# Performance work log

Hardware: AMD Instinct MI355X
Metric: run time of the kernel (lower is better)

## Reference

```python
import jax, jax.numpy as jnp
import numpy as np

D = 256; NH = 8; NL = 4; NP = 4; HD = D // NH
SHAPES = np.array([[64, 64], [32, 32], [16, 16], [8, 8]], dtype=np.int32)  # (H, W) per level
LSI = np.array([0, 4096, 5120, 5376], dtype=np.int32)
B = 4; LQ = int(SHAPES.prod(axis=1).sum())  # 5440


def setup_inputs() -> dict:
    key = jax.random.key(0)
    ks = jax.random.split(key, 16)
    p = lambda i, shape, s=0.02: jax.random.normal(ks[i], shape, dtype=jnp.float32) * s
    return dict(
        src=jax.random.normal(ks[0], (B, LQ, D), dtype=jnp.float32),
        pos=jax.random.normal(ks[1], (B, LQ, D), dtype=jnp.float32),
        reference_points=jax.random.uniform(ks[2], (B, LQ, NL, 2), dtype=jnp.float32),
        spatial_shapes=jnp.asarray(SHAPES),
        level_start_index=jnp.asarray(LSI),
        Wv=p(3, (D, D)), bv=jnp.zeros((D,), jnp.float32),
        Woff=p(4, (D, NH * NL * NP * 2)), boff=p(5, (NH * NL * NP * 2,)),
        Wattn=p(6, (D, NH * NL * NP)), battn=p(7, (NH * NL * NP,)),
        Wout=p(8, (D, D)), bout=jnp.zeros((D,), jnp.float32),
        g1=jnp.ones((D,), jnp.float32), b1=jnp.zeros((D,), jnp.float32),
        W1=p(9, (D, D)), bb1=jnp.zeros((D,), jnp.float32),
        W2=p(10, (D, D)), bb2=jnp.zeros((D,), jnp.float32),
        g3=jnp.ones((D,), jnp.float32), b3=jnp.zeros((D,), jnp.float32),
    )


def _ln(x, g, b, eps=1e-5):
    m = jnp.mean(x, -1, keepdims=True)
    v = jnp.mean(jnp.square(x - m), -1, keepdims=True)
    return (x - m) * jax.lax.rsqrt(v + eps) * g + b


def _bilinear(vflat, Hl, Wl, loc):
    # vflat: [B, Hl*Wl, nh, hd]; loc: [B, Lq, nh, np, 2] normalized to [0,1]
    # align_corners=False, zero padding (matches F.grid_sample in MSDeformAttn)
    x = loc[..., 0] * Wl - 0.5
    y = loc[..., 1] * Hl - 0.5
    x0 = jnp.floor(x); y0 = jnp.floor(y)
    fx = x - x0; fy = y - y0
    x0 = x0.astype(jnp.int32); y0 = y0.astype(jnp.int32)
    Bb, Lq, nh, npnt = x0.shape
    hd = vflat.shape[-1]
    out = jnp.zeros((Bb, Lq, nh, npnt, hd), vflat.dtype)
    for dy in (0, 1):
        for dx in (0, 1):
            xi = x0 + dx; yi = y0 + dy
            w = (fx if dx else 1.0 - fx) * (fy if dy else 1.0 - fy)
            valid = (xi >= 0) & (xi < Wl) & (yi >= 0) & (yi < Hl)
            idx = jnp.clip(yi, 0, Hl - 1) * Wl + jnp.clip(xi, 0, Wl - 1)  # [B,Lq,nh,np]
            idx = idx.transpose(0, 1, 3, 2).reshape(Bb, Lq * npnt, nh, 1)
            g = jnp.take_along_axis(vflat, idx, axis=1)
            g = g.reshape(Bb, Lq, npnt, nh, hd).transpose(0, 1, 3, 2, 4)
            out = out + g * (w * valid.astype(w.dtype))[..., None]
    return out  # [B, Lq, nh, np, hd]


def _forward(src, pos, reference_points, spatial_shapes, level_start_index,
             Wv, bv, Woff, boff, Wattn, battn, Wout, bout,
             g1, b1, W1, bb1, W2, bb2, g3, b3):
    shapes = np.asarray(spatial_shapes)
    lsi = np.asarray(level_start_index)
    Bq, Lq, Dm = src.shape
    q = src + pos  # with_pos_embed
    value = (src @ Wv + bv).reshape(Bq, Lq, NH, HD)
    off = (q @ Woff + boff).reshape(Bq, Lq, NH, NL, NP, 2)
    aw = jax.nn.softmax((q @ Wattn + battn).reshape(Bq, Lq, NH, NL * NP), axis=-1)
    aw = aw.reshape(Bq, Lq, NH, NL, NP)
    # offset normalizer is (W, H) per level
    norm = jnp.stack([shapes[:, 1].astype(np.float32), shapes[:, 0].astype(np.float32)], axis=-1)
    loc = reference_points[:, :, None, :, None, :] + off / norm[None, None, None, :, None, :]
    attended = jnp.zeros((Bq, Lq, NH, HD), src.dtype)
    for l in range(shapes.shape[0]):
        Hl, Wl = int(shapes[l, 0]), int(shapes[l, 1])
        s = int(lsi[l])
        vflat = value[:, s:s + Hl * Wl]
        sampled = _bilinear(vflat, Hl, Wl, loc[:, :, :, l])  # [B,Lq,nh,np,hd]
        attended = attended + jnp.einsum('blhpd,blhp->blhd', sampled, aw[:, :, :, l])
    src2 = attended.reshape(Bq, Lq, Dm) @ Wout + bout
    # residual + LayerNorm (dropout is identity in eval)
    sxy = _ln(src + src2, g1, b1)
    # FFN (d_ffn == d_model here), residual + LayerNorm
    h = jax.nn.relu(sxy @ W1 + bb1)
    return _ln(sxy + (h @ W2 + bb2), g3, b3)


def reference(src, pos, reference_points, spatial_shapes, level_start_index,
              Wv, bv, Woff, boff, Wattn, battn, Wout, bout,
              g1, b1, W1, bb1, W2, bb2, g3, b3):
    return _forward(src, pos, reference_points, spatial_shapes, level_start_index,
                    Wv, bv, Woff, boff, Wattn, battn, Wout, bout,
                    g1, b1, W1, bb1, W2, bb2, g3, b3)
```

## Files before the change

kernel.cpp:

```cpp
#include <hip/hip_runtime.h>
#include <cstddef>
#include <cstdint>

#define M_TOK 21760
#define LQ_ 5440

typedef __bf16 bf16x8 __attribute__((ext_vector_type(8)));
typedef float f32x4v __attribute__((ext_vector_type(4)));
typedef _Float16 half4v __attribute__((ext_vector_type(4)));
typedef short short4v __attribute__((ext_vector_type(4)));

__device__ __forceinline__ unsigned short f2bf(float f) {
  unsigned u = __builtin_bit_cast(unsigned, f);
  unsigned r = u + 0x7fffu + ((u >> 16) & 1u);
  return (unsigned short)(r >> 16);
}
__device__ __forceinline__ float bflo(unsigned u) {
  return __builtin_bit_cast(float, u << 16);
}
__device__ __forceinline__ float bfhi(unsigned u) {
  return __builtin_bit_cast(float, u & 0xffff0000u);
}

__global__ __launch_bounds__(256) void prep_x(
    const float* __restrict__ src, const float* __restrict__ pos,
    unsigned short* __restrict__ s16, unsigned short* __restrict__ q16)
{
  const int i = blockIdx.x * 256 + threadIdx.x;
  const float4 s = ((const float4*)src)[i];
  const float4 p = ((const float4*)pos)[i];
  ushort4 a, b;
  a.x = f2bf(s.x); a.y = f2bf(s.y); a.z = f2bf(s.z); a.w = f2bf(s.w);
  b.x = f2bf(s.x + p.x); b.y = f2bf(s.y + p.y); b.z = f2bf(s.z + p.z); b.w = f2bf(s.w + p.w);
  ((ushort4*)s16)[i] = a;
  ((ushort4*)q16)[i] = b;
}

__global__ __launch_bounds__(256) void prep_w(
    const float* __restrict__ Wv, const float* __restrict__ Woff,
    const float* __restrict__ Wattn, const float* __restrict__ Wout,
    const float* __restrict__ W1, const float* __restrict__ W2,
    unsigned short* __restrict__ G)
{
  const int gid = blockIdx.x * 256 + threadIdx.x;
  const float* srcs[6] = {Wv, Woff, Wattn, Wout, W1, W2};
  const int starts[7] = {0, 65536, 131072, 163840, 229376, 294912, 360448};
  const int Nn[6] = {256, 256, 128, 256, 256, 256};
  int m = 0;
#pragma unroll
  for (int i = 1; i < 6; ++i) m += (gid >= starts[i]);
  const int local = gid - starts[m];
  const int n = local >> 8;
  const int k = local & 255;
  G[gid] = f2bf(srcs[m][(size_t)k * Nn[m] + n]);
}

__global__ __launch_bounds__(256, 2) void gemm_bf16_k(
    const unsigned short* __restrict__ A, const unsigned short* __restrict__ Wt,
    const float* __restrict__ bias, const float* __restrict__ bias2,
    float* __restrict__ outf, unsigned short* __restrict__ out16,
    int N, int relu)
{
  __shared__ unsigned short As[128 * 64];
  __shared__ unsigned short Bs[128 * 64];
  const int t = threadIdx.x;
  const int lane = t & 63, wave = t >> 6;
  const int wm = wave >> 1, wn = wave & 1;
  const int m0 = blockIdx.x * 128, n0 = blockIdx.y * 128;

  const int lrow = lane >> 3;
  const int pcol = (lane & 7) << 4;
  const int scol = pcol ^ (lrow << 4);

  f32x4v acc[4][4];
#pragma unroll
  for (int i = 0; i < 4; ++i)
#pragma unroll
    for (int j = 0; j < 4; ++j) acc[i][j] = (f32x4v){0.f, 0.f, 0.f, 0.f};

  const int fr = lane & 15;
  const int fkb = (lane >> 4) << 4;

  for (int k0 = 0; k0 < 256; k0 += 64) {
#pragma unroll
    for (int i = 0; i < 4; ++i) {
      const int row = wave * 32 + i * 8 + lrow;
      const unsigned short* g = A + (size_t)(m0 + row) * 256 + k0 + (scol >> 1);
      unsigned short* s = As + (wave * 32 + i * 8) * 64;
      __builtin_amdgcn_global_load_lds(
          (const __attribute__((address_space(1))) void*)g,
          (__attribute__((address_space(3))) void*)s, 16, 0, 0);
    }
#pragma unroll
    for (int i = 0; i < 4; ++i) {
      const int row = wave * 32 + i * 8 + lrow;
      const unsigned short* g = Wt + (size_t)(n0 + row) * 256 + k0 + (scol >> 1);
      unsigned short* s = Bs + (wave * 32 + i * 8) * 64;
      __builtin_amdgcn_global_load_lds(
          (const __attribute__((address_space(1))) void*)g,
          (__attribute__((address_space(3))) void*)s, 16, 0, 0);
    }
    __syncthreads();

    bf16x8 af[4][2], bfr[4][2];
#pragma unroll
    for (int i = 0; i < 4; ++i) {
      const int row = wm * 64 + i * 16 + fr;
      const char* base = (const char*)As + row * 128;
#pragma unroll
      for (int kk = 0; kk < 2; ++kk) {
        const int colb = (kk * 64 + fkb) ^ ((row & 7) << 4);
        af[i][kk] = *(const bf16x8*)(base + colb);
      }
    }
#pragma unroll
    for (int j = 0; j < 4; ++j) {
      const int row = wn * 64 + j * 16 + fr;
      const char* base = (const char*)Bs + row * 128;
#pragma unroll
      for (int kk = 0; kk < 2; ++kk) {
        const int colb = (kk * 64 + fkb) ^ ((row & 7) << 4);
        bfr[j][kk] = *(const bf16x8*)(base + colb);
      }
    }
#pragma unroll
    for (int i = 0; i < 4; ++i)
#pragma unroll
      for (int j = 0; j < 4; ++j) {
        acc[i][j] = __builtin_amdgcn_mfma_f32_16x16x32_bf16(af[i][0], bfr[j][0], acc[i][j], 0, 0, 0);
        acc[i][j] = __builtin_amdgcn_mfma_f32_16x16x32_bf16(af[i][1], bfr[j][1], acc[i][j], 0, 0, 0);
      }
    __syncthreads();
  }

  const float* bsel = bias;
  int nsub = 0;
  if (bias2 && n0 >= 256) { bsel = bias2; nsub = 256; }

  const int fq = lane >> 4;
#pragma unroll
  for (int j = 0; j < 4; ++j) {
    const int n = n0 + wn * 64 + j * 16 + fr;
    const float bj = bsel[n - nsub];
#pragma unroll
    for (int i = 0; i < 4; ++i) {
#pragma unroll
      for (int r = 0; r < 4; ++r) {
        const int m = m0 + wm * 64 + i * 16 + fq * 4 + r;
        float v = acc[i][j][r] + bj;
        if (relu) v = fmaxf(v, 0.f);
        if (outf) outf[(size_t)m * N + n] = v;
        if (out16) out16[(size_t)m * N + n] = f2bf(v);
      }
    }
  }
}

__global__ __launch_bounds__(512, 4) void gemm_ln_k(
    const unsigned short* __restrict__ A, const unsigned short* __restrict__ Wt,
    const float* __restrict__ bias, const float* __restrict__ res,
    const float* __restrict__ g, const float* __restrict__ b,
    float* __restrict__ outf, unsigned short* __restrict__ out16)
{
  __shared__ unsigned short As[32 * 64];
  __shared__ unsigned short Bs[256 * 64 + 288];
  const int t = threadIdx.x;
  const int lane = t & 63, wave = t >> 6;
  const int rt = wave & 1, cg = wave >> 1;
  const int m0 = blockIdx.x * 32;

  const int lrow = lane >> 3;
  const int pcol = (lane & 7) << 4;
  const int scol = pcol ^ (lrow << 4);

  f32x4v acc[4];
#pragma unroll
  for (int j = 0; j < 4; ++j) acc[j] = (f32x4v){0.f, 0.f, 0.f, 0.f};

  const int fr = lane & 15;
  const int fq = lane >> 4;
  const int fkb = fq << 4;

  for (int k0 = 0; k0 < 256; k0 += 64) {
    if (wave < 4) {
      const int row = wave * 8 + lrow;
      const unsigned short* gp = A + (size_t)(m0 + row) * 256 + k0 + (scol >> 1);
      unsigned short* s = As + (wave * 8) * 64;
      __builtin_amdgcn_global_load_lds(
          (const __attribute__((address_space(1))) void*)gp,
          (__attribute__((address_space(3))) void*)s, 16, 0, 0);
    }
#pragma unroll
    for (int i = 0; i < 4; ++i) {
      const int row = wave * 32 + i * 8 + lrow;
      const unsigned short* gp = Wt + (size_t)row * 256 + k0 + (scol >> 1);
      unsigned short* s = Bs + (wave * 32 + i * 8) * 64;
      __builtin_amdgcn_global_load_lds(
          (const __attribute__((address_space(1))) void*)gp,
          (__attribute__((address_space(3))) void*)s, 16, 0, 0);
    }
    __syncthreads();

    bf16x8 af0, af1;
    {
      const int arow = rt * 16 + fr;
      const char* abase = (const char*)As + arow * 128;
      af0 = *(const bf16x8*)(abase + ((0 + fkb) ^ ((arow & 7) << 4)));
      af1 = *(const bf16x8*)(abase + ((64 + fkb) ^ ((arow & 7) << 4)));
    }
#pragma unroll
    for (int j = 0; j < 4; ++j) {
      const int brow = cg * 64 + j * 16 + fr;
      const char* bbase = (const char*)Bs + brow * 128;
      const bf16x8 b0 = *(const bf16x8*)(bbase + ((0 + fkb) ^ ((brow & 7) << 4)));
      const bf16x8 b1 = *(const bf16x8*)(bbase + ((64 + fkb) ^ ((brow & 7) << 4)));
      acc[j] = __builtin_amdgcn_mfma_f32_16x16x32_bf16(af0, b0, acc[j], 0, 0, 0);
      acc[j] = __builtin_amdgcn_mfma_f32_16x16x32_bf16(af1, b1, acc[j], 0, 0, 0);
    }
    __syncthreads();
  }

  float* Cs = (float*)Bs;
#pragma unroll
  for (int j = 0; j < 4; ++j) {
    const int col = cg * 64 + j * 16 + fr;
#pragma unroll
    for (int rr = 0; rr < 4; ++rr) {
      const int row = rt * 16 + fq * 4 + rr;
      Cs[row * 260 + col] = acc[j][rr];
    }
  }
  __syncthreads();

  const int lg = lane >> 4, li = lane & 15;
  const int row = wave * 4 + lg;
  const size_t rowoff = (size_t)(m0 + row) * 256;

  float4 v[4];
  float s = 0.f;
#pragma unroll
  for (int c4 = 0; c4 < 4; ++c4) {
    const int col = c4 * 64 + li * 4;
    float4 x = *(float4*)&Cs[row * 260 + col];
    const float4 bi = *(const float4*)&bias[col];
    const float4 rv = *(const float4*)&res[rowoff + col];
    x.x += bi.x + rv.x; x.y += bi.y + rv.y;
    x.z += bi.z + rv.z; x.w += bi.w + rv.w;
    v[c4] = x;
    s += x.x + x.y + x.z + x.w;
  }
#pragma unroll
  for (int o = 1; o < 16; o <<= 1) s += __shfl_xor(s, o);
  const float mean = s * (1.f / 256.f);
  float ss = 0.f;
#pragma unroll
  for (int c4 = 0; c4 < 4; ++c4) {
    const float d0 = v[c4].x - mean, d1 = v[c4].y - mean;
    const float d2 = v[c4].z - mean, d3 = v[c4].w - mean;
    ss += d0 * d0 + d1 * d1 + d2 * d2 + d3 * d3;
  }
#pragma unroll
  for (int o = 1; o < 16; o <<= 1) ss += __shfl_xor(ss, o);
  const float rstd = rsqrtf(ss * (1.f / 256.f) + 1e-5f);

#pragma unroll
  for (int c4 = 0; c4 < 4; ++c4) {
    const int col = c4 * 64 + li * 4;
    const float4 gv = *(const float4*)&g[col];
    const float4 bv = *(const float4*)&b[col];
    float4 o4;
    o4.x = (v[c4].x - mean) * rstd * gv.x + bv.x;
    o4.y = (v[c4].y - mean) * rstd * gv.y + bv.y;
    o4.z = (v[c4].z - mean) * rstd * gv.z + bv.z;
    o4.w = (v[c4].w - mean) * rstd * gv.w + bv.w;
    if (outf) *(float4*)(outf + rowoff + col) = o4;
    if (out16) {
      ushort4 o;
      o.x = f2bf(o4.x); o.y = f2bf(o4.y); o.z = f2bf(o4.z); o.w = f2bf(o4.w);
      *(ushort4*)(out16 + rowoff + col) = o;
    }
  }
}

__global__ __launch_bounds__(256) void samp_k(
    const unsigned short* __restrict__ value16, const float* __restrict__ fused,
    const float* __restrict__ ref, unsigned short* __restrict__ att16)
{
  const int tok0 = blockIdx.x * 8;
  __shared__ half4v  swv[8][136];
  __shared__ short4v siv[8][136];
  const int t = threadIdx.x;

#pragma unroll
  for (int it = 0; it < 4; ++it) {
    const int idx = it * 256 + t;
    const int ti = idx >> 7;
    const int e  = idx & 127;
    const int tok = tok0 + ti;
    const int h = e >> 4;
    const int lvl = (e >> 2) & 3;
    const int HW[4] = {64, 32, 16, 8};
    const int LS[4] = {0, 4096, 5120, 5376};
    const int Wl = HW[lvl];

    const float lg = fused[(size_t)tok * 384 + 256 + e];
    float mx = lg;
#pragma unroll
    for (int o = 1; o < 16; o <<= 1) mx = fmaxf(mx, __shfl_xor(mx, o, 16));
    const float ex = __expf(lg - mx);
    float sm = ex;
#pragma unroll
    for (int o = 1; o < 16; o <<= 1) sm += __shfl_xor(sm, o, 16);
    const float a = ex / sm;

    const float ox = fused[(size_t)tok * 384 + e * 2 + 0];
    const float oy = fused[(size_t)tok * 384 + e * 2 + 1];
    const float rx = ref[(size_t)tok * 8 + lvl * 2 + 0];
    const float ry = ref[(size_t)tok * 8 + lvl * 2 + 1];
    const float x = rx * (float)Wl + ox - 0.5f;
    const float y = ry * (float)Wl + oy - 0.5f;
    const float x0f = floorf(x), y0f = floorf(y);
    const float fx = x - x0f, fy = y - y0f;
    const int x0 = (int)x0f, y0 = (int)y0f;

    const int xi1 = x0 + 1, yi1 = y0 + 1;
    const float wx0 = 1.f - fx, wx1 = fx, wy0 = 1.f - fy, wy1 = fy;
    const int xc0 = min(max(x0, 0), Wl - 1), xc1 = min(max(xi1, 0), Wl - 1);
    const int yc0 = min(max(y0, 0), Wl - 1), yc1 = min(max(yi1, 0), Wl - 1);
    const bool vx0 = (x0 >= 0) & (x0 < Wl), vx1 = (xi1 >= 0) & (xi1 < Wl);
    const bool vy0 = (y0 >= 0) & (y0 < Wl), vy1 = (yi1 >= 0) & (yi1 < Wl);
    half4v hw;
    hw.x = (_Float16)((vx0 & vy0) ? a * wx0 * wy0 : 0.f);
    hw.y = (_Float16)((vx1 & vy0) ? a * wx1 * wy0 : 0.f);
    hw.z = (_Float16)((vx0 & vy1) ? a * wx0 * wy1 : 0.f);
    hw.w = (_Float16)((vx1 & vy1) ? a * wx1 * wy1 : 0.f);
    short4v hs;
    hs.x = (short)(LS[lvl] + yc0 * Wl + xc0);
    hs.y = (short)(LS[lvl] + yc0 * Wl + xc1);
    hs.z = (short)(LS[lvl] + yc1 * Wl + xc0);
    hs.w = (short)(LS[lvl] + yc1 * Wl + xc1);
    const int sl = e + h;
    swv[ti][sl] = hw;
    siv[ti][sl] = hs;
  }
  __syncthreads();

  const int wave = t >> 6, lane = t & 63;
  const int ti = wave * 2 + (lane >> 5);
  const int h = (lane >> 2) & 7, dg = lane & 3;
  const int tok = tok0 + ti;
  const int vbase = (tok / LQ_) * LQ_;
  const unsigned short* vb = value16 + (size_t)vbase * 256 + h * 32 + dg * 8;
  float acc[8] = {0.f, 0.f, 0.f, 0.f, 0.f, 0.f, 0.f, 0.f};
  const int ebase = h * 17;

#pragma unroll 4
  for (int p = 0; p < 16; ++p) {
    const half4v hw = swv[ti][ebase + p];
    const short4v hs = siv[ti][ebase + p];
    const float w0 = (float)hw.x, w1 = (float)hw.y, w2 = (float)hw.z, w3 = (float)hw.w;
    const uint4 u0 = *(const uint4*)(vb + (size_t)(int)hs.x * 256);
    const uint4 u1 = *(const uint4*)(vb + (size_t)(int)hs.y * 256);
    const uint4 u2 = *(const uint4*)(vb + (size_t)(int)hs.z * 256);
    const uint4 u3 = *(const uint4*)(vb + (size_t)(int)hs.w * 256);
#define ACC4(U, W)                                            \
    acc[0] = fmaf(W, bflo(U.x), acc[0]);                      \
    acc[1] = fmaf(W, bfhi(U.x), acc[1]);                      \
    acc[2] = fmaf(W, bflo(U.y), acc[2]);                      \
    acc[3] = fmaf(W, bfhi(U.y), acc[3]);                      \
    acc[4] = fmaf(W, bflo(U.z), acc[4]);                      \
    acc[5] = fmaf(W, bfhi(U.z), acc[5]);                      \
    acc[6] = fmaf(W, bflo(U.w), acc[6]);                      \
    acc[7] = fmaf(W, bfhi(U.w), acc[7]);
    ACC4(u0, w0) ACC4(u1, w1) ACC4(u2, w2) ACC4(u3, w3)
#undef ACC4
  }

  uint4 o;
  o.x = (unsigned)f2bf(acc[0]) | ((unsigned)f2bf(acc[1]) << 16);
  o.y = (unsigned)f2bf(acc[2]) | ((unsigned)f2bf(acc[3]) << 16);
  o.z = (unsigned)f2bf(acc[4]) | ((unsigned)f2bf(acc[5]) << 16);
  o.w = (unsigned)f2bf(acc[6]) | ((unsigned)f2bf(acc[7]) << 16);
  *(uint4*)(att16 + (size_t)tok * 256 + h * 32 + dg * 8) = o;
}

extern "C" void kernel_launch(void* const* d_in, const int* in_sizes, int n_in,
                              void* d_out, int out_size, void* d_ws, size_t ws_size,
                              hipStream_t stream)
{
  const float* src   = (const float*)d_in[0];
  const float* pos   = (const float*)d_in[1];
  const float* ref   = (const float*)d_in[2];
  const float* Wv    = (const float*)d_in[5];
  const float* bv    = (const float*)d_in[6];
  const float* Woff  = (const float*)d_in[7];
  const float* boff  = (const float*)d_in[8];
  const float* Wattn = (const float*)d_in[9];
  const float* battn = (const float*)d_in[10];
  const float* Wout  = (const float*)d_in[11];
  const float* bout  = (const float*)d_in[12];
  const float* g1    = (const float*)d_in[13];
  const float* b1    = (const float*)d_in[14];
  const float* W1    = (const float*)d_in[15];
  const float* bb1   = (const float*)d_in[16];
  const float* W2    = (const float*)d_in[17];
  const float* bb2   = (const float*)d_in[18];
  const float* g3    = (const float*)d_in[19];
  const float* b3    = (const float*)d_in[20];

  float* out = (float*)d_out;
  char* ws = (char*)d_ws;
  const size_t M = M_TOK;

  float* bufA = (float*)ws;
  float* bufB = (float*)(ws + M * 256 * 4);
  unsigned short* bufE = (unsigned short*)(ws + M * 256 * 4 + M * 384 * 4);
  unsigned short* bufF = bufE + M * 256;
  unsigned short* bufG = bufF + M * 256;
  unsigned short* value16 = (unsigned short*)bufA;

  unsigned short* WvT     = bufG + 0;
  unsigned short* WfusedT = bufG + 65536;
  unsigned short* WoutT   = bufG + 163840;
  unsigned short* W1T     = bufG + 229376;
  unsigned short* W2T     = bufG + 294912;

  const dim3 blk(256);

  prep_x<<<dim3(5440), blk, 0, stream>>>(src, pos, bufE, bufF);
  prep_w<<<dim3(1408), blk, 0, stream>>>(Wv, Woff, Wattn, Wout, W1, W2, bufG);

  gemm_bf16_k<<<dim3(170, 2), blk, 0, stream>>>(bufE, WvT, bv, nullptr, nullptr, value16, 256, 0);
  gemm_bf16_k<<<dim3(170, 3), blk, 0, stream>>>(bufF, WfusedT, boff, battn, bufB, nullptr, 384, 0);
  samp_k<<<dim3(2720), blk, 0, stream>>>(value16, bufB, ref, bufE);
  gemm_ln_k<<<dim3(680), dim3(512), 0, stream>>>(bufE, WoutT, bout, src, g1, b1, bufA, bufF);
  gemm_bf16_k<<<dim3(170, 2), blk, 0, stream>>>(bufF, W1T, bb1, nullptr, nullptr, bufE, 256, 1);
  gemm_ln_k<<<dim3(680), dim3(512), 0, stream>>>(bufE, W2T, bb2, bufA, g3, b3, out, nullptr);
}
```

Baseline: 123.2 us.

## Fuse value and offset GEMMs into one launch and switch intermediates to fp16

Merges the value projection and the offset/attention-logit projection into a single GEMM launch selected by blockIdx.y. The offset/logit output is stored as fp16 instead of fp32, halving its write and read traffic. All bf16 storage and MFMA paths are switched to fp16. This reduces launch count, improves occupancy, and cuts memory traffic for the sampling kernel's inputs, at the cost of fp16 range and precision risk for offsets and logits.

```diff
diff --git a/kernel.cpp b/kernel.cpp
--- a/kernel.cpp
+++ b/kernel.cpp
@@ -5,21 +5,18 @@
 #define M_TOK 21760
 #define LQ_ 5440
 
-typedef __bf16 bf16x8 __attribute__((ext_vector_type(8)));
+typedef _Float16 f16x8 __attribute__((ext_vector_type(8)));
+typedef _Float16 h2v __attribute__((ext_vector_type(2)));
 typedef float f32x4v __attribute__((ext_vector_type(4)));
 typedef _Float16 half4v __attribute__((ext_vector_type(4)));
 typedef short short4v __attribute__((ext_vector_type(4)));
 
-__device__ __forceinline__ unsigned short f2bf(float f) {
-  unsigned u = __builtin_bit_cast(unsigned, f);
-  unsigned r = u + 0x7fffu + ((u >> 16) & 1u);
-  return (unsigned short)(r >> 16);
-}
-__device__ __forceinline__ float bflo(unsigned u) {
-  return __builtin_bit_cast(float, u << 16);
-}
-__device__ __forceinline__ float bfhi(unsigned u) {
-  return __builtin_bit_cast(float, u & 0xffff0000u);
+__device__ __forceinline__ unsigned short f2h(float f) {
+  return __builtin_bit_cast(unsigned short, (_Float16)f);
+}
+__device__ __forceinline__ unsigned pack2h(float a, float b) {
+  h2v p; p[0] = (_Float16)a; p[1] = (_Float16)b;
+  return __builtin_bit_cast(unsigned, p);
 }
 
 __global__ __launch_bounds__(256) void prep_x(
@@ -30,8 +27,8 @@
   const float4 s = ((const float4*)src)[i];
   const float4 p = ((const float4*)pos)[i];
   ushort4 a, b;
-  a.x = f2bf(s.x); a.y = f2bf(s.y); a.z = f2bf(s.z); a.w = f2bf(s.w);
-  b.x = f2bf(s.x + p.x); b.y = f2bf(s.y + p.y); b.z = f2bf(s.z + p.z); b.w = f2bf(s.w + p.w);
+  a.x = f2h(s.x); a.y = f2h(s.y); a.z = f2h(s.z); a.w = f2h(s.w);
+  b.x = f2h(s.x + p.x); b.y = f2h(s.y + p.y); b.z = f2h(s.z + p.z); b.w = f2h(s.w + p.w);
   ((ushort4*)s16)[i] = a;
   ((ushort4*)q16)[i] = b;
 }
@@ -52,13 +49,115 @@
   const int local = gid - starts[m];
   const int n = local >> 8;
   const int k = local & 255;
-  G[gid] = f2bf(srcs[m][(size_t)k * Nn[m] + n]);
-}
-
-__global__ __launch_bounds__(256, 2) void gemm_bf16_k(
+  G[gid] = f2h(srcs[m][(size_t)k * Nn[m] + n]);
+}
+
+__global__ __launch_bounds__(256, 2) void gemm_qkv_k(
+    const unsigned short* __restrict__ s16, const unsigned short* __restrict__ q16,
+    const unsigned short* __restrict__ WvT, const unsigned short* __restrict__ WfT,
+    const float* __restrict__ bv, const float* __restrict__ boff,
+    const float* __restrict__ battn,
+    unsigned short* __restrict__ value16, unsigned short* __restrict__ fused16)
+{
+  const int by = blockIdx.y;
+  const bool isv = (by < 2);
+  const unsigned short* A  = isv ? s16 : q16;
+  const unsigned short* Wt = isv ? WvT : WfT;
+  const int n0 = isv ? by * 128 : (by - 2) * 128;
+  const int N  = isv ? 256 : 384;
+  unsigned short* out16 = isv ? value16 : fused16;
+  const float* bsel; int nsub;
+  if (isv)            { bsel = bv;    nsub = 0; }
+  else if (n0 < 256)  { bsel = boff;  nsub = 0; }
+  else                { bsel = battn; nsub = 256; }
+
+  __shared__ unsigned short As[128 * 64];
+  __shared__ unsigned short Bs[128 * 64];
+  const int t = threadIdx.x;
+  const int lane = t & 63, wave = t >> 6;
+  const int wm = wave >> 1, wn = wave & 1;
+  const int m0 = blockIdx.x * 128;
+
+  const int lrow = lane >> 3;
+  const int pcol = (lane & 7) << 4;
+  const int scol = pcol ^ (lrow << 4);
+
+  f32x4v acc[4][4];
+#pragma unroll
+  for (int i = 0; i < 4; ++i)
+#pragma unroll
+    for (int j = 0; j < 4; ++j) acc[i][j] = (f32x4v){0.f, 0.f, 0.f, 0.f};
+
+  const int fr = lane & 15;
+  const int fkb = (lane >> 4) << 4;
+
+  for (int k0 = 0; k0 < 256; k0 += 64) {
+#pragma unroll
+    for (int i = 0; i < 4; ++i) {
+      const int row = wave * 32 + i * 8 + lrow;
+      const unsigned short* g = A + (size_t)(m0 + row) * 256 + k0 + (scol >> 1);
+      unsigned short* s = As + (wave * 32 + i * 8) * 64;
+      __builtin_amdgcn_global_load_lds(
+          (const __attribute__((address_space(1))) void*)g,
+          (__attribute__((address_space(3))) void*)s, 16, 0, 0);
+    }
+#pragma unroll
+    for (int i = 0; i < 4; ++i) {
+      const int row = wave * 32 + i * 8 + lrow;
+      const unsigned short* g = Wt + (size_t)(n0 + row) * 256 + k0 + (scol >> 1);
+      unsigned short* s = Bs + (wave * 32 + i * 8) * 64;
+      __builtin_amdgcn_global_load_lds(
+          (const __attribute__((address_space(1))) void*)g,
+          (__attribute__((address_space(3))) void*)s, 16, 0, 0);
+    }
+    __syncthreads();
+
+    f16x8 af[4][2], bfr[4][2];
+#pragma unroll
+    for (int i = 0; i < 4; ++i) {
+      const int row = wm * 64 + i * 16 + fr;
+      const char* base = (const char*)As + row * 128;
+#pragma unroll
+      for (int kk = 0; kk < 2; ++kk)
+        af[i][kk] = *(const f16x8*)(base + ((kk * 64 + fkb) ^ ((row & 7) << 4)));
+    }
+#pragma unroll
+    for (int j = 0; j < 4; ++j) {
+      const int row = wn * 64 + j * 16 + fr;
+      const char* base = (const char*)Bs + row * 128;
+#pragma unroll
+      for (int kk = 0; kk < 2; ++kk)
+        bfr[j][kk] = *(const f16x8*)(base + ((kk * 64 + fkb) ^ ((row & 7) << 4)));
+    }
+#pragma unroll
+    for (int i = 0; i < 4; ++i)
+#pragma unroll
+      for (int j = 0; j < 4; ++j) {
+        acc[i][j] = __builtin_amdgcn_mfma_f32_16x16x32_f16(af[i][0], bfr[j][0], acc[i][j], 0, 0, 0);
+        acc[i][j] = __builtin_amdgcn_mfma_f32_16x16x32_f16(af[i][1], bfr[j][1], acc[i][j], 0, 0, 0);
+      }
+    __syncthreads();
+  }
+
+  const int fq = lane >> 4;
+#pragma unroll
+  for (int j = 0; j < 4; ++j) {
+    const int n = n0 + wn * 64 + j * 16 + fr;
+    const float bj = bsel[n - nsub];
+#pragma unroll
+    for (int i = 0; i < 4; ++i) {
+#pragma unroll
+      for (int r = 0; r < 4; ++r) {
+        const int m = m0 + wm * 64 + i * 16 + fq * 4 + r;
+        out16[(size_t)m * N + n] = f2h(acc[i][j][r] + bj);
+      }
+    }
+  }
+}
+
+__global__ __launch_bounds__(256, 2) void gemm16_k(
     const unsigned short* __restrict__ A, const unsigned short* __restrict__ Wt,
-    const float* __restrict__ bias, const float* __restrict__ bias2,
-    float* __restrict__ outf, unsigned short* __restrict__ out16,
+    const float* __restrict__ bias, unsigned short* __restrict__ out16,
     int N, int relu)
 {
   __shared__ unsigned short As[128 * 64];
@@ -102,46 +201,38 @@
     }
     __syncthreads();
 
-    bf16x8 af[4][2], bfr[4][2];
+    f16x8 af[4][2], bfr[4][2];
 #pragma unroll
     for (int i = 0; i < 4; ++i) {
       const int row = wm * 64 + i * 16 + fr;
       const char* base = (const char*)As + row * 128;
 #pragma unroll
-      for (int kk = 0; kk < 2; ++kk) {
-        const int colb = (kk * 64 + fkb) ^ ((row & 7) << 4);
-        af[i][kk] = *(const bf16x8*)(base + colb);
-      }
+      for (int kk = 0; kk < 2; ++kk)
+        af[i][kk] = *(const f16x8*)(base + ((kk * 64 + fkb) ^ ((row & 7) << 4)));
     }
 #pragma unroll
     for (int j = 0; j < 4; ++j) {
       const int row = wn * 64 + j * 16 + fr;
       const char* base = (const char*)Bs + row * 128;
 #pragma unroll
-      for (int kk = 0; kk < 2; ++kk) {
-        const int colb = (kk * 64 + fkb) ^ ((row & 7) << 4);
-        bfr[j][kk] = *(const bf16x8*)(base + colb);
-      }
+      for (int kk = 0; kk < 2; ++kk)
+        bfr[j][kk] = *(const f16x8*)(base + ((kk * 64 + fkb) ^ ((row & 7) << 4)));
     }
 #pragma unroll
     for (int i = 0; i < 4; ++i)
 #pragma unroll
       for (int j = 0; j < 4; ++j) {
-        acc[i][j] = __builtin_amdgcn_mfma_f32_16x16x32_bf16(af[i][0], bfr[j][0], acc[i][j], 0, 0, 0);
-        acc[i][j] = __builtin_amdgcn_mfma_f32_16x16x32_bf16(af[i][1], bfr[j][1], acc[i][j], 0, 0, 0);
+        acc[i][j] = __builtin_amdgcn_mfma_f32_16x16x32_f16(af[i][0], bfr[j][0], acc[i][j], 0, 0, 0);
+        acc[i][j] = __builtin_amdgcn_mfma_f32_16x16x32_f16(af[i][1], bfr[j][1], acc[i][j], 0, 0, 0);
       }
     __syncthreads();
   }
 
-  const float* bsel = bias;
-  int nsub = 0;
-  if (bias2 && n0 >= 256) { bsel = bias2; nsub = 256; }
-
   const int fq = lane >> 4;
 #pragma unroll
   for (int j = 0; j < 4; ++j) {
     const int n = n0 + wn * 64 + j * 16 + fr;
-    const float bj = bsel[n - nsub];
+    const float bj = bias[n];
 #pragma unroll
     for (int i = 0; i < 4; ++i) {
 #pragma unroll
@@ -149,8 +240,7 @@
         const int m = m0 + wm * 64 + i * 16 + fq * 4 + r;
         float v = acc[i][j][r] + bj;
         if (relu) v = fmaxf(v, 0.f);
-        if (outf) outf[(size_t)m * N + n] = v;
-        if (out16) out16[(size_t)m * N + n] = f2bf(v);
+        out16[(size_t)m * N + n] = f2h(v);
       }
     }
   }
@@ -201,21 +291,21 @@
     }
     __syncthreads();
 
-    bf16x8 af0, af1;
+    f16x8 af0, af1;
     {
       const int arow = rt * 16 + fr;
       const char* abase = (const char*)As + arow * 128;
-      af0 = *(const bf16x8*)(abase + ((0 + fkb) ^ ((arow & 7) << 4)));
-      af1 = *(const bf16x8*)(abase + ((64 + fkb) ^ ((arow & 7) << 4)));
+      af0 = *(const f16x8*)(abase + ((0 + fkb) ^ ((arow & 7) << 4)));
+      af1 = *(const f16x8*)(abase + ((64 + fkb) ^ ((arow & 7) << 4)));
     }
 #pragma unroll
     for (int j = 0; j < 4; ++j) {
       const int brow = cg * 64 + j * 16 + fr;
       const char* bbase = (const char*)Bs + brow * 128;
-      const bf16x8 b0 = *(const bf16x8*)(bbase + ((0 + fkb) ^ ((brow & 7) << 4)));
-      const bf16x8 b1 = *(const bf16x8*)(bbase + ((64 + fkb) ^ ((brow & 7) << 4)));
-      acc[j] = __builtin_amdgcn_mfma_f32_16x16x32_bf16(af0, b0, acc[j], 0, 0, 0);
-      acc[j] = __builtin_amdgcn_mfma_f32_16x16x32_bf16(af1, b1, acc[j], 0, 0, 0);
+      const f16x8 b0 = *(const f16x8*)(bbase + ((0 + fkb) ^ ((brow & 7) << 4)));
+      const f16x8 b1 = *(const f16x8*)(bbase + ((64 + fkb) ^ ((brow & 7) << 4)));
+      acc[j] = __builtin_amdgcn_mfma_f32_16x16x32_f16(af0, b0, acc[j], 0, 0, 0);
+      acc[j] = __builtin_amdgcn_mfma_f32_16x16x32_f16(af1, b1, acc[j], 0, 0, 0);
     }
     __syncthreads();
   }
@@ -276,20 +366,21 @@
     if (outf) *(float4*)(outf + rowoff + col) = o4;
     if (out16) {
       ushort4 o;
-      o.x = f2bf(o4.x); o.y = f2bf(o4.y); o.z = f2bf(o4.z); o.w = f2bf(o4.w);
+      o.x = f2h(o4.x); o.y = f2h(o4.y); o.z = f2h(o4.z); o.w = f2h(o4.w);
       *(ushort4*)(out16 + rowoff + col) = o;
     }
   }
 }
 
 __global__ __launch_bounds__(256) void samp_k(
-    const unsigned short* __restrict__ value16, const float* __restrict__ fused,
+    const unsigned short* __restrict__ value16, const unsigned short* __restrict__ fused16,
     const float* __restrict__ ref, unsigned short* __restrict__ att16)
 {
   const int tok0 = blockIdx.x * 8;
   __shared__ half4v  swv[8][136];
   __shared__ short4v siv[8][136];
   const int t = threadIdx.x;
+  const _Float16* fh = (const _Float16*)fused16;
 
 #pragma unroll
   for (int it = 0; it < 4; ++it) {
@@ -303,7 +394,7 @@
     const int LS[4] = {0, 4096, 5120, 5376};
     const int Wl = HW[lvl];
 
-    const float lg = fused[(size_t)tok * 384 + 256 + e];
+    const float lg = (float)fh[(size_t)tok * 384 + 256 + e];
     float mx = lg;
 #pragma unroll
     for (int o = 1; o < 16; o <<= 1) mx = fmaxf(mx, __shfl_xor(mx, o, 16));
@@ -313,8 +404,8 @@
     for (int o = 1; o < 16; o <<= 1) sm += __shfl_xor(sm, o, 16);
     const float a = ex / sm;
 
-    const float ox = fused[(size_t)tok * 384 + e * 2 + 0];
-    const float oy = fused[(size_t)tok * 384 + e * 2 + 1];
+    const float ox = (float)fh[(size_t)tok * 384 + e * 2 + 0];
+    const float oy = (float)fh[(size_t)tok * 384 + e * 2 + 1];
     const float rx = ref[(size_t)tok * 8 + lvl * 2 + 0];
     const float ry = ref[(size_t)tok * 8 + lvl * 2 + 1];
     const float x = rx * (float)Wl + ox - 0.5f;
@@ -363,24 +454,28 @@
     const uint4 u1 = *(const uint4*)(vb + (size_t)(int)hs.y * 256);
     const uint4 u2 = *(const uint4*)(vb + (size_t)(int)hs.z * 256);
     const uint4 u3 = *(const uint4*)(vb + (size_t)(int)hs.w * 256);
-#define ACC4(U, W)                                            \
-    acc[0] = fmaf(W, bflo(U.x), acc[0]);                      \
-    acc[1] = fmaf(W, bfhi(U.x), acc[1]);                      \
-    acc[2] = fmaf(W, bflo(U.y), acc[2]);                      \
-    acc[3] = fmaf(W, bfhi(U.y), acc[3]);                      \
-    acc[4] = fmaf(W, bflo(U.z), acc[4]);                      \
-    acc[5] = fmaf(W, bfhi(U.z), acc[5]);                      \
-    acc[6] = fmaf(W, bflo(U.w), acc[6]);                      \
-    acc[7] = fmaf(W, bfhi(U.w), acc[7]);
+#define ACC4(U, W) {                                              \
+    const h2v p0 = __builtin_bit_cast(h2v, U.x);                  \
+    const h2v p1 = __builtin_bit_cast(h2v, U.y);                  \
+    const h2v p2 = __builtin_bit_cast(h2v, U.z);                  \
+    const h2v p3 = __builtin_bit_cast(h2v, U.w);                  \
+    acc[0] = fmaf(W, (float)p0[0], acc[0]);                       \
+    acc[1] = fmaf(W, (float)p0[1], acc[1]);                       \
+    acc[2] = fmaf(W, (float)p1[0], acc[2]);                       \
+    acc[3] = fmaf(W, (float)p1[1], acc[3]);                       \
+    acc[4] = fmaf(W, (float)p2[0], acc[4]);                       \
+    acc[5] = fmaf(W, (float)p2[1], acc[5]);                       \
+    acc[6] = fmaf(W, (float)p3[0], acc[6]);                       \
+    acc[7] = fmaf(W, (float)p3[1], acc[7]); }
     ACC4(u0, w0) ACC4(u1, w1) ACC4(u2, w2) ACC4(u3, w3)
 #undef ACC4
   }
 
   uint4 o;
-  o.x = (unsigned)f2bf(acc[0]) | ((unsigned)f2bf(acc[1]) << 16);
-  o.y = (unsigned)f2bf(acc[2]) | ((unsigned)f2bf(acc[3]) << 16);
-  o.z = (unsigned)f2bf(acc[4]) | ((unsigned)f2bf(acc[5]) << 16);
-  o.w = (unsigned)f2bf(acc[6]) | ((unsigned)f2bf(acc[7]) << 16);
+  o.x = pack2h(acc[0], acc[1]);
+  o.y = pack2h(acc[2], acc[3]);
+  o.z = pack2h(acc[4], acc[5]);
+  o.w = pack2h(acc[6], acc[7]);
   *(uint4*)(att16 + (size_t)tok * 256 + h * 32 + dg * 8) = o;
 }
 
@@ -413,8 +508,8 @@
   const size_t M = M_TOK;
 
   float* bufA = (float*)ws;
-  float* bufB = (float*)(ws + M * 256 * 4);
-  unsigned short* bufE = (unsigned short*)(ws + M * 256 * 4 + M * 384 * 4);
+  unsigned short* fused16 = (unsigned short*)(ws + M * 256 * 4);
+  unsigned short* bufE = fused16 + M * 384;
   unsigned short* bufF = bufE + M * 256;
   unsigned short* bufG = bufF + M * 256;
   unsigned short* value16 = (unsigned short*)bufA;
@@ -430,10 +525,10 @@
   prep_x<<<dim3(5440), blk, 0, stream>>>(src, pos, bufE, bufF);
   prep_w<<<dim3(1408), blk, 0, stream>>>(Wv, Woff, Wattn, Wout, W1, W2, bufG);
 
-  gemm_bf16_k<<<dim3(170, 2), blk, 0, stream>>>(bufE, WvT, bv, nullptr, nullptr, value16, 256, 0);
-  gemm_bf16_k<<<dim3(170, 3), blk, 0, stream>>>(bufF, WfusedT, boff, battn, bufB, nullptr, 384, 0);
-  samp_k<<<dim3(2720), blk, 0, stream>>>(value16, bufB, ref, bufE);
+  gemm_qkv_k<<<dim3(170, 5), blk, 0, stream>>>(bufE, bufF, WvT, WfusedT,
+                                               bv, boff, battn, value16, fused16);
+  samp_k<<<dim3(2720), blk, 0, stream>>>(value16, fused16, ref, bufE);
   gemm_ln_k<<<dim3(680), dim3(512), 0, stream>>>(bufE, WoutT, bout, src, g1, b1, bufA, bufF);
-  gemm_bf16_k<<<dim3(170, 2), blk, 0, stream>>>(bufF, W1T, bb1, nullptr, nullptr, bufE, 256, 1);
+  gemm16_k<<<dim3(170, 2), blk, 0, stream>>>(bufF, W1T, bb1, bufE, 256, 1);
   gemm_ln_k<<<dim3(680), dim3(512), 0, stream>>>(bufE, W2T, bb2, bufA, g3, b3, out, nullptr);
 }
```

After: 117.0 us. 1.05x faster.
